# Optimization experiments

Hardware: AMD Instinct MI355X
Metric: run time of the kernel (lower is better)

Reference implementation:

```python
import jax, jax.numpy as jnp
import numpy as np

SEQ_LEN, BZ, D_IN = 512, 64, 1024
HIDDEN, D_OUT, NUM_LANG = 256, 1024, 16


def setup_inputs() -> dict:
    key = jax.random.key(0)
    ks = jax.random.split(key, 6)
    x = jax.random.normal(ks[0], (SEQ_LEN, BZ, D_IN), dtype=jnp.float32)
    lang_ids = jax.random.randint(ks[1], (BZ,), 0, NUM_LANG, dtype=jnp.int64)
    # Per-language 2-layer MLP params, stacked over the language axis.
    # Stored as [in, out] so y = x @ W + b (same math as torch Linear's x @ W.T + b).
    s1 = 1.0 / np.sqrt(D_IN)
    s2 = 1.0 / np.sqrt(HIDDEN)
    W1 = jax.random.uniform(ks[2], (NUM_LANG, D_IN, HIDDEN), jnp.float32, -s1, s1)
    b1 = jax.random.uniform(ks[3], (NUM_LANG, HIDDEN), jnp.float32, -s1, s1)
    W2 = jax.random.uniform(ks[4], (NUM_LANG, HIDDEN, D_OUT), jnp.float32, -s2, s2)
    b2 = jax.random.uniform(ks[5], (NUM_LANG, D_OUT), jnp.float32, -s2, s2)
    return {"x": x, "lang_ids": lang_ids, "W1": W1, "b1": b1, "W2": W2, "b2": b2}


def reference(x, lang_ids, W1, b1, W2, b2):
    # Gather each batch element's expert weights, then do batched GEMMs.
    # Equivalent to the torch loop (dispatch -> per-expert MLP -> combine),
    # without redundant gather/scatter passes.
    W1g = W1[lang_ids]            # [bz, d_in, hidden]
    b1g = b1[lang_ids]            # [bz, hidden]
    W2g = W2[lang_ids]            # [bz, hidden, d_out]
    b2g = b2[lang_ids]            # [bz, d_out]
    h = jnp.einsum('sbd,bdh->sbh', x, W1g) + b1g[None, :, :]
    h = jax.nn.relu(h)
    y = jnp.einsum('sbh,bho->sbo', h, W2g) + b2g[None, :, :]
    return y
```

## Files before the change

kernel.cpp:

```cpp
#include <hip/hip_runtime.h>

#define SEQ 512
#define BZ  64
#define DIN 1024
#define HID 256
#define DOUT 1024
#define NLANG 16

typedef __attribute__((ext_vector_type(8))) __bf16 bf16x8;
typedef __attribute__((ext_vector_type(4))) float f32x4;

__device__ __forceinline__ unsigned short f2bf(float f) {
    return __builtin_bit_cast(unsigned short, (__bf16)f);
}
__device__ __forceinline__ unsigned int f2bf_pack(float lo, float hi) {
    return (unsigned int)f2bf(lo) | ((unsigned int)f2bf(hi) << 16);
}
__device__ __forceinline__ void gload_lds16(const void* g, void* l) {
    __builtin_amdgcn_global_load_lds(
        (const __attribute__((address_space(1))) unsigned int*)g,
        (__attribute__((address_space(3))) unsigned int*)l, 16, 0, 0);
}

template<int K, int N>
__global__ __launch_bounds__(256)
void prep_frags(const float* __restrict__ src, unsigned short* __restrict__ dst) {
    constexpr int K32 = K / 32, N16 = N / 16;
    const int gid = blockIdx.x * 256 + threadIdx.x;
    const int l   = gid & 63;
    const int f   = gid >> 6;
    const int k32 = f & (K32 - 1);
    const int n16 = (f / K32) & (N16 - 1);
    const int lid = f / (K32 * N16);
    const float* s = src + ((long)lid * K + k32 * 32 + (l >> 4) * 8) * N + n16 * 16 + (l & 15);
    unsigned short o[8];
#pragma unroll
    for (int j = 0; j < 8; ++j) o[j] = f2bf(s[(long)j * N]);
    uint4 v;
    v.x = (unsigned int)o[0] | ((unsigned int)o[1] << 16);
    v.y = (unsigned int)o[2] | ((unsigned int)o[3] << 16);
    v.z = (unsigned int)o[4] | ((unsigned int)o[5] << 16);
    v.w = (unsigned int)o[6] | ((unsigned int)o[7] << 16);
    *(uint4*)(dst + (long)gid * 8) = v;
}

__global__ __launch_bounds__(512, 2)
void mlp_l1(const float* __restrict__ x,
            const unsigned short* __restrict__ W1f,
            const float* __restrict__ b1,
            const int* __restrict__ lang,
            unsigned short* __restrict__ h_ws) {
    __shared__ float sX[2][64 * 64];
    __shared__ unsigned short sH[64 * 256];
    char* cH = (char*)sH;

    const int b  = blockIdx.x;
    const int st = blockIdx.y;
    const int t  = threadIdx.x;
    const int l  = t & 63;
    const int w  = t >> 6;
    const int lid = lang[b];
    const long xstride = (long)BZ * DIN;
    const float* xb = x + (long)(st * 64) * xstride + (long)b * DIN;

    const float* gsrc[2];
#pragma unroll
    for (int j = 0; j < 2; ++j) {
        int r = (w * 2 + j) * 4 + (l >> 4);
        int c = (l & 15) ^ (r & 15);
        gsrc[j] = xb + (long)r * xstride + c * 4;
    }
#define STAGE(KT, BUF)                                                            \
    {                                                                             \
        _Pragma("unroll")                                                         \
        for (int j = 0; j < 2; ++j)                                               \
            gload_lds16(gsrc[j] + (KT) * 64,                                      \
                        (char*)sX[BUF] + (w * 2 + j) * 1024);                     \
    }

    const f32x4 z4 = {0.f, 0.f, 0.f, 0.f};
    f32x4 acc1[4][2];
#pragma unroll
    for (int mi = 0; mi < 4; ++mi)
#pragma unroll
        for (int ni = 0; ni < 2; ++ni) acc1[mi][ni] = z4;

    const unsigned short* w1p = W1f + (((long)lid * 16 + w * 2) * 32) * 512 + (long)l * 8;

    float bvv[2];
#pragma unroll
    for (int ni = 0; ni < 2; ++ni)
        bvv[ni] = b1[lid * HID + w * 32 + ni * 16 + (l & 15)];

    STAGE(0, 0);
    bf16x8 bvp[2][2];
#pragma unroll
    for (int ni = 0; ni < 2; ++ni)
        bvp[0][ni] = __builtin_bit_cast(bf16x8, *(const uint4*)(w1p + (long)ni * 16384));
    __syncthreads();

    for (int kt = 0; kt < 16; ++kt) {
        if (kt < 15) STAGE(kt + 1, (kt + 1) & 1);
        const char* cX = (const char*)sX[kt & 1];
#pragma unroll
        for (int ks = 0; ks < 2; ++ks) {
            const int p = kt * 2 + ks;
            if (p < 31) {
#pragma unroll
                for (int ni = 0; ni < 2; ++ni)
                    bvp[(p + 1) & 1][ni] = __builtin_bit_cast(bf16x8,
                        *(const uint4*)(w1p + (long)ni * 16384 + (p + 1) * 512));
            }
            bf16x8 av[4];
#pragma unroll
            for (int mi = 0; mi < 4; ++mi) {
                const int r  = mi * 16 + (l & 15);
                const int c0 = ks * 8 + (l >> 4) * 2;
                const char* base = cX + r * 256;
                const float4 v0 = *(const float4*)(base + ((c0 ^ (r & 15)) << 4));
                const float4 v1 = *(const float4*)(base + (((c0 + 1) ^ (r & 15)) << 4));
                uint4 pk;
                pk.x = f2bf_pack(v0.x, v0.y);
                pk.y = f2bf_pack(v0.z, v0.w);
                pk.z = f2bf_pack(v1.x, v1.y);
                pk.w = f2bf_pack(v1.z, v1.w);
                av[mi] = __builtin_bit_cast(bf16x8, pk);
            }
#pragma unroll
            for (int mi = 0; mi < 4; ++mi)
#pragma unroll
                for (int ni = 0; ni < 2; ++ni)
                    acc1[mi][ni] = __builtin_amdgcn_mfma_f32_16x16x32_bf16(
                        av[mi], bvp[p & 1][ni], acc1[mi][ni], 0, 0, 0);
        }
        __syncthreads();
    }

#pragma unroll
    for (int mi = 0; mi < 4; ++mi)
#pragma unroll
        for (int r = 0; r < 4; ++r) {
            int row = mi * 16 + (l >> 4) * 4 + r;
#pragma unroll
            for (int ni = 0; ni < 2; ++ni) {
                int col = w * 32 + ni * 16 + (l & 15);
                float v = acc1[mi][ni][r] + bvv[ni];
                v = v > 0.f ? v : 0.f;
                *(unsigned short*)(cH + row * 512 + (((col >> 3) ^ (row & 7)) << 4)
                                   + (col & 7) * 2) = f2bf(v);
            }
        }
    __syncthreads();

    uint4* hw = (uint4*)(h_ws + ((long)(b * 8 + st)) * 16384);
    const uint4* sq = (const uint4*)sH;
#pragma unroll
    for (int j = 0; j < 4; ++j)
        hw[t + 512 * j] = sq[t + 512 * j];
#undef STAGE
}

__global__ __launch_bounds__(512, 2)
void mlp_l2(const unsigned short* __restrict__ h_ws,
            const unsigned short* __restrict__ W2f,
            const float* __restrict__ b2,
            const int* __restrict__ lang,
            float* __restrict__ y) {
    __shared__ unsigned short sH[64 * 256];
    char* cH = (char*)sH;

    const int b  = blockIdx.x;
    const int st = blockIdx.y;
    const int t  = threadIdx.x;
    const int l  = t & 63;
    const int w  = t >> 6;
    const int lid = lang[b];
    const int s0  = st * 64;

    const unsigned short* hw = h_ws + ((long)(b * 8 + st)) * 16384;
#pragma unroll
    for (int j = 0; j < 4; ++j) {
        int seg = w * 4 + j;
        gload_lds16(hw + seg * 512 + l * 8, sH + seg * 512);
    }

    const unsigned short* w2p = W2f + (((long)lid * 64 + w * 8) * 8) * 512 + (long)l * 8;

    const f32x4 z4 = {0.f, 0.f, 0.f, 0.f};
    bf16x8 pv[2][4];
#pragma unroll
    for (int ni = 0; ni < 4; ++ni)
        pv[0][ni] = __builtin_bit_cast(bf16x8, *(const uint4*)(w2p + (long)ni * 4096));

    __syncthreads();

    f32x4 acc[4][4];
    float b2v[4];
#pragma unroll
    for (int s = 0; s < 16; ++s) {
        const int nc = s >> 3, ks = s & 7, cur = s & 1;
        if (ks == 0) {
#pragma unroll
            for (int mi = 0; mi < 4; ++mi)
#pragma unroll
                for (int ni = 0; ni < 4; ++ni) acc[mi][ni] = z4;
#pragma unroll
            for (int ni = 0; ni < 4; ++ni)
                b2v[ni] = b2[lid * DOUT + w * 128 + nc * 64 + ni * 16 + (l & 15)];
        }
        if (s < 15) {
            const int ns = s + 1, nq = (ns >> 3) * 4, ks1 = ns & 7;
#pragma unroll
            for (int ni = 0; ni < 4; ++ni)
                pv[cur ^ 1][ni] = __builtin_bit_cast(bf16x8,
                    *(const uint4*)(w2p + (long)(nq + ni) * 4096 + ks1 * 512));
        }
        bf16x8 av2[4];
#pragma unroll
        for (int mi = 0; mi < 4; ++mi) {
            int row = mi * 16 + (l & 15);
            int ch  = ks * 4 + (l >> 4);
            av2[mi] = __builtin_bit_cast(bf16x8,
                *(const uint4*)(cH + row * 512 + ((ch ^ (row & 7)) << 4)));
        }
#pragma unroll
        for (int mi = 0; mi < 4; ++mi)
#pragma unroll
            for (int ni = 0; ni < 4; ++ni)
                acc[mi][ni] = __builtin_amdgcn_mfma_f32_16x16x32_bf16(
                    av2[mi], pv[cur][ni], acc[mi][ni], 0, 0, 0);
        if (ks == 7) {
#pragma unroll
            for (int mi = 0; mi < 4; ++mi)
#pragma unroll
                for (int r = 0; r < 4; ++r) {
                    int row = mi * 16 + (l >> 4) * 4 + r;
#pragma unroll
                    for (int ni = 0; ni < 4; ++ni) {
                        int col = w * 128 + nc * 64 + ni * 16 + (l & 15);
                        y[((long)(s0 + row) * BZ + b) * DOUT + col] =
                            acc[mi][ni][r] + b2v[ni];
                    }
                }
        }
    }
}

extern "C" void kernel_launch(void* const* d_in, const int* in_sizes, int n_in,
                              void* d_out, int out_size, void* d_ws, size_t ws_size,
                              hipStream_t stream) {
    const float* x    = (const float*)d_in[0];
    const int*   lang = (const int*)d_in[1];
    const float* W1   = (const float*)d_in[2];
    const float* b1   = (const float*)d_in[3];
    const float* W2   = (const float*)d_in[4];
    const float* b2   = (const float*)d_in[5];
    float* y = (float*)d_out;

    unsigned short* W1f = (unsigned short*)d_ws;
    unsigned short* W2f = (unsigned short*)((char*)d_ws + (size_t)NLANG * HID * DIN * 2);
    unsigned short* hws = (unsigned short*)((char*)d_ws + (size_t)NLANG * HID * DIN * 2
                                                       + (size_t)NLANG * DOUT * HID * 2);

    prep_frags<DIN, HID><<<2048, 256, 0, stream>>>(W1, W1f);
    prep_frags<HID, DOUT><<<2048, 256, 0, stream>>>(W2, W2f);

    mlp_l1<<<dim3(BZ, SEQ / 64), 512, 0, stream>>>(x, W1f, b1, lang, hws);
    mlp_l2<<<dim3(BZ, SEQ / 64), 512, 0, stream>>>(hws, W2f, b2, lang, y);
}
```

Measured before the change: 107.6 us.

## Retile layer-1 GEMM to 16-row blocks grouped by language for W1 cache reuse

The layer-1 kernel now handles 16 sequence rows per block instead of 64, which launches 2048 blocks instead of 512. It loads the whole 16x1024 x tile into LDS in one shot, replacing the double-buffered k-loop. Blocks are also remapped through a language-sorted rank of batch elements, with an XCD-aware interleave, so blocks sharing a W1 expert land close together and reuse it in L2. The cost is that each block reads the full W1 slice for only 16 rows, so W1 fragment traffic from L2 is four times higher. Each wave also issues fewer MFMAs per weight load, and every block recomputes the 64x64 rank sort.

```diff
diff --git a/kernel.cpp b/kernel.cpp
--- a/kernel.cpp
+++ b/kernel.cpp
@@ -50,114 +50,101 @@
             const float* __restrict__ b1,
             const int* __restrict__ lang,
             unsigned short* __restrict__ h_ws) {
-    __shared__ float sX[2][64 * 64];
-    __shared__ unsigned short sH[64 * 256];
+    __shared__ float sX[16 * 1024];
+    __shared__ unsigned short sH[16 * 256];
+    __shared__ int rank_to_b[64];
+    char* cX = (char*)sX;
     char* cH = (char*)sH;
 
-    const int b  = blockIdx.x;
-    const int st = blockIdx.y;
     const int t  = threadIdx.x;
     const int l  = t & 63;
-    const int w  = t >> 6;
-    const int lid = lang[b];
+    const int wv = t >> 6;
+
+    if (t < 64) {
+        const int my = lang[t];
+        int rank = 0;
+        for (int b2 = 0; b2 < 64; ++b2) {
+            const int lb = lang[b2];
+            rank += (lb < my) || (lb == my && b2 < t);
+        }
+        rank_to_b[rank] = t;
+    }
+    __syncthreads();
+
+    const int id   = blockIdx.x;
+    const int pos  = (id & 7) * 256 + (id >> 3);
+    const int b    = rank_to_b[pos >> 5];
+    const int st16 = pos & 31;
+    const int lid  = lang[b];
     const long xstride = (long)BZ * DIN;
-    const float* xb = x + (long)(st * 64) * xstride + (long)b * DIN;
-
-    const float* gsrc[2];
-#pragma unroll
-    for (int j = 0; j < 2; ++j) {
-        int r = (w * 2 + j) * 4 + (l >> 4);
-        int c = (l & 15) ^ (r & 15);
-        gsrc[j] = xb + (long)r * xstride + c * 4;
-    }
-#define STAGE(KT, BUF)                                                            \
-    {                                                                             \
-        _Pragma("unroll")                                                         \
-        for (int j = 0; j < 2; ++j)                                               \
-            gload_lds16(gsrc[j] + (KT) * 64,                                      \
-                        (char*)sX[BUF] + (w * 2 + j) * 1024);                     \
-    }
-
-    const f32x4 z4 = {0.f, 0.f, 0.f, 0.f};
-    f32x4 acc1[4][2];
-#pragma unroll
-    for (int mi = 0; mi < 4; ++mi)
-#pragma unroll
-        for (int ni = 0; ni < 2; ++ni) acc1[mi][ni] = z4;
-
-    const unsigned short* w1p = W1f + (((long)lid * 16 + w * 2) * 32) * 512 + (long)l * 8;
+    const float* xb = x + (long)(st16 * 16) * xstride + (long)b * DIN;
+
+#pragma unroll
+    for (int j = 0; j < 8; ++j) {
+        const int q = t + j * 512;
+        const int r = q >> 8, c = q & 255;
+        gload_lds16(xb + (long)r * xstride + (long)(c ^ (r & 15)) * 4,
+                    cX + (wv * 64 + j * 512) * 16);
+    }
+
+    const unsigned short* w1p = W1f + (((long)lid * 16 + wv * 2) * 32) * 512 + (long)l * 8;
 
     float bvv[2];
 #pragma unroll
     for (int ni = 0; ni < 2; ++ni)
-        bvv[ni] = b1[lid * HID + w * 32 + ni * 16 + (l & 15)];
-
-    STAGE(0, 0);
+        bvv[ni] = b1[lid * HID + (wv * 2 + ni) * 16 + (l & 15)];
+
     bf16x8 bvp[2][2];
 #pragma unroll
     for (int ni = 0; ni < 2; ++ni)
         bvp[0][ni] = __builtin_bit_cast(bf16x8, *(const uint4*)(w1p + (long)ni * 16384));
-    __syncthreads();
-
-    for (int kt = 0; kt < 16; ++kt) {
-        if (kt < 15) STAGE(kt + 1, (kt + 1) & 1);
-        const char* cX = (const char*)sX[kt & 1];
-#pragma unroll
-        for (int ks = 0; ks < 2; ++ks) {
-            const int p = kt * 2 + ks;
-            if (p < 31) {
-#pragma unroll
-                for (int ni = 0; ni < 2; ++ni)
-                    bvp[(p + 1) & 1][ni] = __builtin_bit_cast(bf16x8,
-                        *(const uint4*)(w1p + (long)ni * 16384 + (p + 1) * 512));
-            }
-            bf16x8 av[4];
-#pragma unroll
-            for (int mi = 0; mi < 4; ++mi) {
-                const int r  = mi * 16 + (l & 15);
-                const int c0 = ks * 8 + (l >> 4) * 2;
-                const char* base = cX + r * 256;
-                const float4 v0 = *(const float4*)(base + ((c0 ^ (r & 15)) << 4));
-                const float4 v1 = *(const float4*)(base + (((c0 + 1) ^ (r & 15)) << 4));
-                uint4 pk;
-                pk.x = f2bf_pack(v0.x, v0.y);
-                pk.y = f2bf_pack(v0.z, v0.w);
-                pk.z = f2bf_pack(v1.x, v1.y);
-                pk.w = f2bf_pack(v1.z, v1.w);
-                av[mi] = __builtin_bit_cast(bf16x8, pk);
-            }
-#pragma unroll
-            for (int mi = 0; mi < 4; ++mi)
-#pragma unroll
-                for (int ni = 0; ni < 2; ++ni)
-                    acc1[mi][ni] = __builtin_amdgcn_mfma_f32_16x16x32_bf16(
-                        av[mi], bvp[p & 1][ni], acc1[mi][ni], 0, 0, 0);
-        }
-        __syncthreads();
-    }
-
-#pragma unroll
-    for (int mi = 0; mi < 4; ++mi)
-#pragma unroll
-        for (int r = 0; r < 4; ++r) {
-            int row = mi * 16 + (l >> 4) * 4 + r;
-#pragma unroll
-            for (int ni = 0; ni < 2; ++ni) {
-                int col = w * 32 + ni * 16 + (l & 15);
-                float v = acc1[mi][ni][r] + bvv[ni];
-                v = v > 0.f ? v : 0.f;
-                *(unsigned short*)(cH + row * 512 + (((col >> 3) ^ (row & 7)) << 4)
-                                   + (col & 7) * 2) = f2bf(v);
-            }
-        }
-    __syncthreads();
-
-    uint4* hw = (uint4*)(h_ws + ((long)(b * 8 + st)) * 16384);
-    const uint4* sq = (const uint4*)sH;
-#pragma unroll
-    for (int j = 0; j < 4; ++j)
-        hw[t + 512 * j] = sq[t + 512 * j];
-#undef STAGE
+
+    const f32x4 z4 = {0.f, 0.f, 0.f, 0.f};
+    f32x4 acc[2] = {z4, z4};
+
+    __syncthreads();
+
+    const int r  = l & 15;
+    const char* rbase = cX + r * 4096;
+#pragma unroll
+    for (int kk = 0; kk < 32; ++kk) {
+        if (kk < 31) {
+#pragma unroll
+            for (int ni = 0; ni < 2; ++ni)
+                bvp[(kk + 1) & 1][ni] = __builtin_bit_cast(bf16x8,
+                    *(const uint4*)(w1p + (long)ni * 16384 + (kk + 1) * 512));
+        }
+        const int c0 = kk * 8 + (l >> 4) * 2;
+        const float4 v0 = *(const float4*)(rbase + ((c0 ^ r) << 4));
+        const float4 v1 = *(const float4*)(rbase + (((c0 + 1) ^ r) << 4));
+        uint4 pk;
+        pk.x = f2bf_pack(v0.x, v0.y);
+        pk.y = f2bf_pack(v0.z, v0.w);
+        pk.z = f2bf_pack(v1.x, v1.y);
+        pk.w = f2bf_pack(v1.z, v1.w);
+        const bf16x8 av = __builtin_bit_cast(bf16x8, pk);
+#pragma unroll
+        for (int ni = 0; ni < 2; ++ni)
+            acc[ni] = __builtin_amdgcn_mfma_f32_16x16x32_bf16(
+                av, bvp[kk & 1][ni], acc[ni], 0, 0, 0);
+    }
+
+#pragma unroll
+    for (int ni = 0; ni < 2; ++ni)
+#pragma unroll
+        for (int rr = 0; rr < 4; ++rr) {
+            const int row = (l >> 4) * 4 + rr;
+            const int col = (wv * 2 + ni) * 16 + (l & 15);
+            float v = acc[ni][rr] + bvv[ni];
+            v = v > 0.f ? v : 0.f;
+            *(unsigned short*)(cH + row * 512 + (((col >> 3) ^ (row & 7)) << 4)
+                               + (col & 7) * 2) = f2bf(v);
+        }
+    __syncthreads();
+
+    uint4* hw = (uint4*)(h_ws + ((long)(b * 8 + (st16 >> 2))) * 16384
+                              + (long)(st16 & 3) * 4096);
+    hw[t] = ((const uint4*)sH)[t];
 }
 
 __global__ __launch_bounds__(512, 2)
@@ -265,6 +252,6 @@
     prep_frags<DIN, HID><<<2048, 256, 0, stream>>>(W1, W1f);
     prep_frags<HID, DOUT><<<2048, 256, 0, stream>>>(W2, W2f);
 
-    mlp_l1<<<dim3(BZ, SEQ / 64), 512, 0, stream>>>(x, W1f, b1, lang, hws);
+    mlp_l1<<<dim3(BZ * (SEQ / 16)), 512, 0, stream>>>(x, W1f, b1, lang, hws);
     mlp_l2<<<dim3(BZ, SEQ / 64), 512, 0, stream>>>(hws, W2f, b2, lang, y);
 }
```

New measurement: 125.3 us. +16.4%, slower.
